# Performance work log

Measured on AMD Instinct MI355X. Metric: run time of the kernel, lower is better.

The kernel has to match this reference:

```python
import jax, jax.numpy as jnp
import numpy as np

N = 200000
E = 3200000
NHID = 128
NUM_GRAPHS = 512


def setup_inputs() -> dict:
    key = jax.random.key(0)
    k_x, k_ei, k_b, k_n, k_w1, k_w2, k_bl = jax.random.split(key, 7)
    x = jax.random.normal(k_x, (N, NHID), dtype=jnp.float32)
    edge_index = jax.random.randint(k_ei, (2, E), 0, N, dtype=jnp.int32)
    batch = jnp.sort(jax.random.randint(k_b, (N,), 0, NUM_GRAPHS, dtype=jnp.int32))
    noise = jax.random.normal(k_n, (N, NHID), dtype=jnp.float32)
    # Generator params (xavier-ish init)
    h = NHID // 2
    W1 = jax.random.normal(k_w1, (NHID, h), dtype=jnp.float32) * np.float32(1.0 / np.sqrt(NHID))
    b1 = jnp.zeros((h,), dtype=jnp.float32)
    W2 = jax.random.normal(k_w2, (h, NHID), dtype=jnp.float32) * np.float32(1.0 / np.sqrt(h))
    b2 = jnp.zeros((NHID,), dtype=jnp.float32)
    return {"x": x, "edge_index": edge_index, "batch": batch, "noise": noise,
            "W1": W1, "b1": b1, "W2": W2, "b2": b2}


def scatter_mean(src_feats, dst_idx, num_nodes):
    # sum messages per destination node, then divide by in-degree (clamped to 1)
    summed = jax.ops.segment_sum(src_feats, dst_idx, num_segments=num_nodes)
    counts = jax.ops.segment_sum(jnp.ones((src_feats.shape[0],), src_feats.dtype),
                                 dst_idx, num_segments=num_nodes)
    return summed / jnp.maximum(counts, 1.0)[:, None]


def reference(x, edge_index, batch, noise, W1, b1, W2, b2):
    src, dst = edge_index[0], edge_index[1]
    # NeighborPropagate: mean aggregation of x_j = x[src] at dst
    x_neighbor = scatter_mean(x[src], dst, x.shape[0])  # [N, nhid]
    g = x_neighbor + noise
    # Generator MLP: relu(fc2(relu(fc1(g))))
    h = jax.nn.relu(g @ W1 + b1)
    x_gen = jax.nn.relu(h @ W2 + b2)
    return x_gen
```

## Files before the change

### kernel.cpp

```cpp
#include <hip/hip_runtime.h>

#define NHID 128
#define HDIM 64
#define EPB 4096
#define MAXBKT 1024
#define CAP 6144

typedef __attribute__((ext_vector_type(8))) short bf16x8;
typedef __attribute__((ext_vector_type(4))) float f32x4;

__device__ __forceinline__ unsigned short f2bf_rn(float f) {
    union { float f; unsigned u; } c; c.f = f;
    unsigned r = c.u + 0x7fffu + ((c.u >> 16) & 1u);
    return (unsigned short)(r >> 16);
}
__device__ __forceinline__ float bf_lo(unsigned d) {
    union { unsigned u; float f; } c; c.u = d << 16; return c.f;
}
__device__ __forceinline__ float bf_hi(unsigned d) {
    union { unsigned u; float f; } c; c.u = d & 0xFFFF0000u; return c.f;
}

__global__ __launch_bounds__(256) void prep_bf16(const float* __restrict__ x,
                                                 unsigned short* __restrict__ xh,
                                                 long long total8) {
    long long t = (long long)blockIdx.x * blockDim.x + threadIdx.x;
    if (t >= total8) return;
    const float4 a = *(const float4*)(x + t * 8);
    const float4 b = *(const float4*)(x + t * 8 + 4);
    ushort4 p, q;
    p.x = f2bf_rn(a.x); p.y = f2bf_rn(a.y); p.z = f2bf_rn(a.z); p.w = f2bf_rn(a.w);
    q.x = f2bf_rn(b.x); q.y = f2bf_rn(b.y); q.z = f2bf_rn(b.z); q.w = f2bf_rn(b.w);
    *(ushort4*)(xh + t * 8) = p;
    *(ushort4*)(xh + t * 8 + 4) = q;
}

__global__ __launch_bounds__(256) void bucket_scatter(const int* __restrict__ src,
                                                      const int* __restrict__ dst,
                                                      int* __restrict__ bucket_cursor,
                                                      unsigned int* __restrict__ bpack,
                                                      int E, int NBKT) {
    __shared__ int h[MAXBKT];
    int t = threadIdx.x;
    long long base = (long long)blockIdx.x * EPB;
    for (int i = t; i < NBKT; i += 256) h[i] = 0;
    __syncthreads();
    for (int p = 0; p < EPB / 256; ++p) {
        long long e = base + p * 256 + t;
        if (e < E) atomicAdd(&h[((unsigned)dst[e]) >> 8], 1);
    }
    __syncthreads();
    for (int i = t; i < NBKT; i += 256) {
        int c = h[i];
        h[i] = c ? (i * CAP + atomicAdd(&bucket_cursor[i], c)) : 0;
    }
    __syncthreads();
    for (int p = 0; p < EPB / 256; ++p) {
        long long e = base + p * 256 + t;
        if (e < E) {
            int d = dst[e];
            int s = src[e];
            int b = ((unsigned)d) >> 8;
            int pos = atomicAdd(&h[b], 1);
            if (pos < (b + 1) * CAP)
                bpack[pos] = (((unsigned)d & 255u) << 24) | (unsigned)s;
        }
    }
}

__global__ __launch_bounds__(256) void bucket_build(unsigned int* __restrict__ bpack,
                                                    const int* __restrict__ bucket_cursor,
                                                    int* __restrict__ cnt,
                                                    int* __restrict__ rowptr,
                                                    int N) {
    __shared__ unsigned ebuf[CAP];
    __shared__ int lc[256];
    __shared__ int sc[256];
    int b = blockIdx.x, t = threadIdx.x;
    int beg = b * CAP;
    int m = bucket_cursor[b]; if (m > CAP) m = CAP;
    lc[t] = 0;
    __syncthreads();
    for (int i = t; i < m; i += 256) {
        unsigned v = bpack[beg + i];
        ebuf[i] = v;
        atomicAdd(&lc[v >> 24], 1);
    }
    __syncthreads();
    int myc = lc[t];
    sc[t] = myc; __syncthreads();
    for (int off = 1; off < 256; off <<= 1) {
        int v = (t >= off) ? sc[t - off] : 0;
        __syncthreads();
        sc[t] += v;
        __syncthreads();
    }
    int excl = sc[t] - myc;
    int node = b * 256 + t;
    if (node < N) { cnt[node] = myc; rowptr[node] = beg + excl; }
    lc[t] = excl;
    __syncthreads();
    for (int i = t; i < m; i += 256) {
        unsigned v = ebuf[i];
        int pos = atomicAdd(&lc[v >> 24], 1);
        bpack[beg + pos] = v & 0xFFFFFFu;
    }
}

__global__ __launch_bounds__(256) void gather_bf16(
    const unsigned short* __restrict__ xh, const unsigned int* __restrict__ perm,
    const int* __restrict__ rowptr, const int* __restrict__ cnt,
    float* __restrict__ sums, int N)
{
    long long t = (long long)blockIdx.x * blockDim.x + threadIdx.x;
    int n = (int)(t >> 4);
    int c = (int)(t & 15);
    if (n >= N) return;
    int beg = rowptr[n];
    int deg = cnt[n];
    float a0 = 0.f, a1 = 0.f, a2 = 0.f, a3 = 0.f, a4 = 0.f, a5 = 0.f, a6 = 0.f, a7 = 0.f;
    int i = 0;
    for (; i + 1 < deg; i += 2) {
        unsigned s0 = perm[beg + i];
        unsigned s1 = perm[beg + i + 1];
        uint4 u = *(const uint4*)(xh + (long long)s0 * NHID + c * 8);
        uint4 v = *(const uint4*)(xh + (long long)s1 * NHID + c * 8);
        a0 += bf_lo(u.x) + bf_lo(v.x); a1 += bf_hi(u.x) + bf_hi(v.x);
        a2 += bf_lo(u.y) + bf_lo(v.y); a3 += bf_hi(u.y) + bf_hi(v.y);
        a4 += bf_lo(u.z) + bf_lo(v.z); a5 += bf_hi(u.z) + bf_hi(v.z);
        a6 += bf_lo(u.w) + bf_lo(v.w); a7 += bf_hi(u.w) + bf_hi(v.w);
    }
    if (i < deg) {
        unsigned s0 = perm[beg + i];
        uint4 u = *(const uint4*)(xh + (long long)s0 * NHID + c * 8);
        a0 += bf_lo(u.x); a1 += bf_hi(u.x);
        a2 += bf_lo(u.y); a3 += bf_hi(u.y);
        a4 += bf_lo(u.z); a5 += bf_hi(u.z);
        a6 += bf_lo(u.w); a7 += bf_hi(u.w);
    }
    float* o = sums + (long long)n * NHID + c * 8;
    float4 r0; r0.x = a0; r0.y = a1; r0.z = a2; r0.w = a3;
    float4 r1; r1.x = a4; r1.y = a5; r1.z = a6; r1.w = a7;
    *(float4*)(o) = r0;
    *(float4*)(o + 4) = r1;
}

__global__ __launch_bounds__(256) void mlp_mfma(
    float* __restrict__ out,
    const int* __restrict__ cnt,
    const float* __restrict__ noise,
    const float* __restrict__ W1, const float* __restrict__ b1,
    const float* __restrict__ W2, const float* __restrict__ b2,
    int N)
{
    __shared__ __align__(16) unsigned short w1t[64 * 136];
    __shared__ __align__(16) unsigned short w2t[128 * 72];
    __shared__ __align__(16) unsigned short ht[4][16 * 72];
    __shared__ float b1s[HDIM];
    __shared__ float b2s[NHID];

    int t = threadIdx.x;
    int wave = t >> 6;
    int lane = t & 63;
    int m = lane & 15;
    int quad = lane >> 4;

    #pragma unroll 4
    for (int p = 0; p < 32; ++p) {
        int idx = p * 256 + t;
        int k = idx >> 6, n = idx & 63;
        w1t[n * 136 + k] = f2bf_rn(W1[idx]);
    }
    #pragma unroll 4
    for (int p = 0; p < 32; ++p) {
        int idx = p * 256 + t;
        int k = idx >> 7, n = idx & 127;
        w2t[n * 72 + k] = f2bf_rn(W2[idx]);
    }
    if (t < HDIM) b1s[t] = b1[t];
    else if (t < HDIM + NHID) b2s[t - HDIM] = b2[t - HDIM];
    __syncthreads();

    int node = blockIdx.x * 64 + wave * 16 + m;
    int nodec = node < N ? node : N - 1;
    float inv = 1.0f / fmaxf((float)cnt[nodec], 1.0f);
    const float* srow = out   + (long long)nodec * NHID;
    const float* nrow = noise + (long long)nodec * NHID;

    bf16x8 afrag[4];
    #pragma unroll
    for (int kc = 0; kc < 4; ++kc) {
        int off = kc * 32 + quad * 8;
        float4 s0 = *(const float4*)(srow + off);
        float4 s1 = *(const float4*)(srow + off + 4);
        float4 n0 = *(const float4*)(nrow + off);
        float4 n1 = *(const float4*)(nrow + off + 4);
        afrag[kc][0] = (short)f2bf_rn(fmaf(s0.x, inv, n0.x));
        afrag[kc][1] = (short)f2bf_rn(fmaf(s0.y, inv, n0.y));
        afrag[kc][2] = (short)f2bf_rn(fmaf(s0.z, inv, n0.z));
        afrag[kc][3] = (short)f2bf_rn(fmaf(s0.w, inv, n0.w));
        afrag[kc][4] = (short)f2bf_rn(fmaf(s1.x, inv, n1.x));
        afrag[kc][5] = (short)f2bf_rn(fmaf(s1.y, inv, n1.y));
        afrag[kc][6] = (short)f2bf_rn(fmaf(s1.z, inv, n1.z));
        afrag[kc][7] = (short)f2bf_rn(fmaf(s1.w, inv, n1.w));
    }

    unsigned short* hw = &ht[wave][0];
    #pragma unroll
    for (int nt = 0; nt < 4; ++nt) {
        f32x4 acc = {0.f, 0.f, 0.f, 0.f};
        #pragma unroll
        for (int kc = 0; kc < 4; ++kc) {
            bf16x8 bfrag = *(const bf16x8*)&w1t[(nt * 16 + m) * 136 + kc * 32 + quad * 8];
            acc = __builtin_amdgcn_mfma_f32_16x16x32_bf16(afrag[kc], bfrag, acc, 0, 0, 0);
        }
        float bb = b1s[nt * 16 + m];
        #pragma unroll
        for (int r = 0; r < 4; ++r) {
            hw[(quad * 4 + r) * 72 + nt * 16 + m] = f2bf_rn(fmaxf(acc[r] + bb, 0.0f));
        }
    }

    bf16x8 a2[2];
    #pragma unroll
    for (int kc = 0; kc < 2; ++kc)
        a2[kc] = *(const bf16x8*)&hw[m * 72 + kc * 32 + quad * 8];

    float* obase = out + ((long long)blockIdx.x * 64 + wave * 16) * NHID;
    #pragma unroll
    for (int nt = 0; nt < 8; ++nt) {
        f32x4 acc = {0.f, 0.f, 0.f, 0.f};
        #pragma unroll
        for (int kc = 0; kc < 2; ++kc) {
            bf16x8 bfrag = *(const bf16x8*)&w2t[(nt * 16 + m) * 72 + kc * 32 + quad * 8];
            acc = __builtin_amdgcn_mfma_f32_16x16x32_bf16(a2[kc], bfrag, acc, 0, 0, 0);
        }
        float bb = b2s[nt * 16 + m];
        #pragma unroll
        for (int r = 0; r < 4; ++r) {
            int orow = blockIdx.x * 64 + wave * 16 + quad * 4 + r;
            if (orow < N)
                obase[(quad * 4 + r) * NHID + nt * 16 + m] = fmaxf(acc[r] + bb, 0.0f);
        }
    }
}

extern "C" void kernel_launch(void* const* d_in, const int* in_sizes, int n_in,
                              void* d_out, int out_size, void* d_ws, size_t ws_size,
                              hipStream_t stream) {
    const float* x     = (const float*)d_in[0];
    const int*   ei    = (const int*)d_in[1];
    const float* noise = (const float*)d_in[3];
    const float* W1    = (const float*)d_in[4];
    const float* b1    = (const float*)d_in[5];
    const float* W2    = (const float*)d_in[6];
    const float* b2    = (const float*)d_in[7];
    float* out = (float*)d_out;

    const int N = in_sizes[2];
    const int E = in_sizes[1] / 2;
    const int* src = ei;
    const int* dst = ei + E;
    const int NBKT = (N + 255) >> 8;

    int* bucket_cursor = (int*)d_ws;
    int* cnt           = bucket_cursor + MAXBKT;
    int* rowptr        = cnt + N;
    unsigned int* bpack = (unsigned int*)(rowptr + N);
    unsigned short* xh  = (unsigned short*)(bpack + (size_t)NBKT * CAP);

    hipMemsetAsync(bucket_cursor, 0, (size_t)MAXBKT * sizeof(int), stream);

    {
        long long total8 = (long long)N * NHID / 8;
        prep_bf16<<<(int)((total8 + 255) / 256), 256, 0, stream>>>(x, xh, total8);
    }
    {
        const int EB = (int)(((long long)E + EPB - 1) / EPB);
        bucket_scatter<<<EB, 256, 0, stream>>>(src, dst, bucket_cursor, bpack, E, NBKT);
    }
    bucket_build<<<NBKT, 256, 0, stream>>>(bpack, bucket_cursor, cnt, rowptr, N);
    {
        long long total = (long long)N * 16;
        gather_bf16<<<(int)((total + 255) / 256), 256, 0, stream>>>(xh, bpack, rowptr, cnt, out, N);
    }
    mlp_mfma<<<(N + 63) / 64, 256, 0, stream>>>(out, cnt, noise, W1, b1, W2, b2, N);
}
```

Measured before the change: 518.3 us.

## Fuse mean-divide and noise add into gather, pass bf16 intermediate to MLP

The gather kernel now divides by degree, adds noise, and writes the bf16 result into the first half of each output row, in place of fp32 sums. The MLP kernel reads these bf16 fragments directly and no longer loads sums, counts or noise. This cuts intermediate traffic between the two kernels, since the MLP reads a quarter of the bytes it did before. The gather loop is also unrolled from two to four edges for more memory-level parallelism. Because the output buffer is aliased and mlp_mfma writes rows in place, correctness depends on each block reading its own rows before overwriting them, which is why __restrict__ was removed.

```diff
diff --git a/kernel.cpp b/kernel.cpp
--- a/kernel.cpp
+++ b/kernel.cpp
@@ -107,10 +107,10 @@
     }
 }
 
-__global__ __launch_bounds__(256) void gather_bf16(
+__global__ __launch_bounds__(256) void gather_fuse(
     const unsigned short* __restrict__ xh, const unsigned int* __restrict__ perm,
     const int* __restrict__ rowptr, const int* __restrict__ cnt,
-    float* __restrict__ sums, int N)
+    const float* __restrict__ noise, unsigned short* __restrict__ g, int N)
 {
     long long t = (long long)blockIdx.x * blockDim.x + threadIdx.x;
     int n = (int)(t >> 4);
@@ -119,36 +119,54 @@
     int beg = rowptr[n];
     int deg = cnt[n];
     float a0 = 0.f, a1 = 0.f, a2 = 0.f, a3 = 0.f, a4 = 0.f, a5 = 0.f, a6 = 0.f, a7 = 0.f;
+    const unsigned short* xb = xh + c * 8;
     int i = 0;
-    for (; i + 1 < deg; i += 2) {
+    for (; i + 3 < deg; i += 4) {
         unsigned s0 = perm[beg + i];
         unsigned s1 = perm[beg + i + 1];
-        uint4 u = *(const uint4*)(xh + (long long)s0 * NHID + c * 8);
-        uint4 v = *(const uint4*)(xh + (long long)s1 * NHID + c * 8);
-        a0 += bf_lo(u.x) + bf_lo(v.x); a1 += bf_hi(u.x) + bf_hi(v.x);
-        a2 += bf_lo(u.y) + bf_lo(v.y); a3 += bf_hi(u.y) + bf_hi(v.y);
-        a4 += bf_lo(u.z) + bf_lo(v.z); a5 += bf_hi(u.z) + bf_hi(v.z);
-        a6 += bf_lo(u.w) + bf_lo(v.w); a7 += bf_hi(u.w) + bf_hi(v.w);
-    }
-    if (i < deg) {
+        unsigned s2 = perm[beg + i + 2];
+        unsigned s3 = perm[beg + i + 3];
+        uint4 u0 = *(const uint4*)(xb + (long long)s0 * NHID);
+        uint4 u1 = *(const uint4*)(xb + (long long)s1 * NHID);
+        uint4 u2 = *(const uint4*)(xb + (long long)s2 * NHID);
+        uint4 u3 = *(const uint4*)(xb + (long long)s3 * NHID);
+        a0 += (bf_lo(u0.x) + bf_lo(u1.x)) + (bf_lo(u2.x) + bf_lo(u3.x));
+        a1 += (bf_hi(u0.x) + bf_hi(u1.x)) + (bf_hi(u2.x) + bf_hi(u3.x));
+        a2 += (bf_lo(u0.y) + bf_lo(u1.y)) + (bf_lo(u2.y) + bf_lo(u3.y));
+        a3 += (bf_hi(u0.y) + bf_hi(u1.y)) + (bf_hi(u2.y) + bf_hi(u3.y));
+        a4 += (bf_lo(u0.z) + bf_lo(u1.z)) + (bf_lo(u2.z) + bf_lo(u3.z));
+        a5 += (bf_hi(u0.z) + bf_hi(u1.z)) + (bf_hi(u2.z) + bf_hi(u3.z));
+        a6 += (bf_lo(u0.w) + bf_lo(u1.w)) + (bf_lo(u2.w) + bf_lo(u3.w));
+        a7 += (bf_hi(u0.w) + bf_hi(u1.w)) + (bf_hi(u2.w) + bf_hi(u3.w));
+    }
+    for (; i < deg; ++i) {
         unsigned s0 = perm[beg + i];
-        uint4 u = *(const uint4*)(xh + (long long)s0 * NHID + c * 8);
+        uint4 u = *(const uint4*)(xb + (long long)s0 * NHID);
         a0 += bf_lo(u.x); a1 += bf_hi(u.x);
         a2 += bf_lo(u.y); a3 += bf_hi(u.y);
         a4 += bf_lo(u.z); a5 += bf_hi(u.z);
         a6 += bf_lo(u.w); a7 += bf_hi(u.w);
     }
-    float* o = sums + (long long)n * NHID + c * 8;
-    float4 r0; r0.x = a0; r0.y = a1; r0.z = a2; r0.w = a3;
-    float4 r1; r1.x = a4; r1.y = a5; r1.z = a6; r1.w = a7;
-    *(float4*)(o) = r0;
-    *(float4*)(o + 4) = r1;
+    float inv = 1.0f / fmaxf((float)deg, 1.0f);
+    const float* nr = noise + (long long)n * NHID + c * 8;
+    float4 n0 = *(const float4*)nr;
+    float4 n1 = *(const float4*)(nr + 4);
+    ushort4 p, q;
+    p.x = f2bf_rn(fmaf(a0, inv, n0.x));
+    p.y = f2bf_rn(fmaf(a1, inv, n0.y));
+    p.z = f2bf_rn(fmaf(a2, inv, n0.z));
+    p.w = f2bf_rn(fmaf(a3, inv, n0.w));
+    q.x = f2bf_rn(fmaf(a4, inv, n1.x));
+    q.y = f2bf_rn(fmaf(a5, inv, n1.y));
+    q.z = f2bf_rn(fmaf(a6, inv, n1.z));
+    q.w = f2bf_rn(fmaf(a7, inv, n1.w));
+    unsigned short* go = g + (long long)n * 256 + c * 8;
+    *(ushort4*)go = p;
+    *(ushort4*)(go + 4) = q;
 }
 
 __global__ __launch_bounds__(256) void mlp_mfma(
-    float* __restrict__ out,
-    const int* __restrict__ cnt,
-    const float* __restrict__ noise,
+    float* out,
     const float* __restrict__ W1, const float* __restrict__ b1,
     const float* __restrict__ W2, const float* __restrict__ b2,
     int N)
@@ -183,27 +201,12 @@
 
     int node = blockIdx.x * 64 + wave * 16 + m;
     int nodec = node < N ? node : N - 1;
-    float inv = 1.0f / fmaxf((float)cnt[nodec], 1.0f);
-    const float* srow = out   + (long long)nodec * NHID;
-    const float* nrow = noise + (long long)nodec * NHID;
-
+
+    const unsigned short* grow = (const unsigned short*)out + (long long)nodec * 256;
     bf16x8 afrag[4];
     #pragma unroll
-    for (int kc = 0; kc < 4; ++kc) {
-        int off = kc * 32 + quad * 8;
-        float4 s0 = *(const float4*)(srow + off);
-        float4 s1 = *(const float4*)(srow + off + 4);
-        float4 n0 = *(const float4*)(nrow + off);
-        float4 n1 = *(const float4*)(nrow + off + 4);
-        afrag[kc][0] = (short)f2bf_rn(fmaf(s0.x, inv, n0.x));
-        afrag[kc][1] = (short)f2bf_rn(fmaf(s0.y, inv, n0.y));
-        afrag[kc][2] = (short)f2bf_rn(fmaf(s0.z, inv, n0.z));
-        afrag[kc][3] = (short)f2bf_rn(fmaf(s0.w, inv, n0.w));
-        afrag[kc][4] = (short)f2bf_rn(fmaf(s1.x, inv, n1.x));
-        afrag[kc][5] = (short)f2bf_rn(fmaf(s1.y, inv, n1.y));
-        afrag[kc][6] = (short)f2bf_rn(fmaf(s1.z, inv, n1.z));
-        afrag[kc][7] = (short)f2bf_rn(fmaf(s1.w, inv, n1.w));
-    }
+    for (int kc = 0; kc < 4; ++kc)
+        afrag[kc] = *(const bf16x8*)(grow + kc * 32 + quad * 8);
 
     unsigned short* hw = &ht[wave][0];
     #pragma unroll
@@ -282,7 +285,8 @@
     bucket_build<<<NBKT, 256, 0, stream>>>(bpack, bucket_cursor, cnt, rowptr, N);
     {
         long long total = (long long)N * 16;
-        gather_bf16<<<(int)((total + 255) / 256), 256, 0, stream>>>(xh, bpack, rowptr, cnt, out, N);
-    }
-    mlp_mfma<<<(N + 63) / 64, 256, 0, stream>>>(out, cnt, noise, W1, b1, W2, b2, N);
-}
+        gather_fuse<<<(int)((total + 255) / 256), 256, 0, stream>>>(
+            xh, bpack, rowptr, cnt, noise, (unsigned short*)out, N);
+    }
+    mlp_mfma<<<(N + 63) / 64, 256, 0, stream>>>(out, W1, b1, W2, b2, N);
+}
```

Measured after the change: 501.7 us. 1.03x faster.
